# Kernel tuning notes

Hardware: AMD Instinct MI355X
Metric: run time of the kernel (lower is better)

The kernel has to match this reference:

```python
import jax, jax.numpy as jnp
import numpy as np

D_K = 64

def setup_inputs() -> dict:
    key = jax.random.key(0)
    kq, kk, kv, km = jax.random.split(key, 4)
    B, H, S, D = 2, 16, 2048, D_K
    q = jax.random.normal(kq, (B, H, S, D), dtype=jnp.float32)
    k = jax.random.normal(kk, (B, H, S, D), dtype=jnp.float32)
    v = jax.random.normal(kv, (B, H, S, D), dtype=jnp.float32)
    atten_mask = jax.random.bernoulli(km, 0.1, (B, H, S, S))  # True = masked out
    return {"q": q, "k": k, "v": v, "atten_mask": atten_mask}

def reference(q, k, v, atten_mask):
    # score = q @ k^T / sqrt(d_k)  -> [B, H, S, S]
    score = jnp.einsum("bhqd,bhkd->bhqk", q, k) / np.sqrt(D_K).astype(np.float32)
    score = jnp.where(atten_mask, jnp.float32(-1e9), score)
    attn = jax.nn.softmax(score, axis=-1)
    return attn  # original module stops before the AV matmul (v unused)
```

## Files before the change

### kernel.cpp

```cpp
#include <hip/hip_runtime.h>

typedef _Float16 f16x8 __attribute__((ext_vector_type(8)));
typedef _Float16 f16x4 __attribute__((ext_vector_type(4)));
typedef float    f32x4 __attribute__((ext_vector_type(4)));
typedef int      i32x4 __attribute__((ext_vector_type(4)));

#define S_LEN 2048
#define D_KH  64
#define NBH   32
#define QTILE 16
#define NBLK  (NBH * (S_LEN / QTILE))
#define THREADS 512
#define QK_ELEMS (NBH * S_LEN * D_KH)

__device__ __forceinline__ f16x8 cvt8(const float4 a, const float4 b) {
  f16x8 r;
  r[0] = (_Float16)a.x; r[1] = (_Float16)a.y;
  r[2] = (_Float16)a.z; r[3] = (_Float16)a.w;
  r[4] = (_Float16)b.x; r[5] = (_Float16)b.y;
  r[6] = (_Float16)b.z; r[7] = (_Float16)b.w;
  return r;
}

__global__ __launch_bounds__(256) void cvt_qk_kernel(
    const float* __restrict__ q, const float* __restrict__ kmat,
    _Float16* __restrict__ qh, _Float16* __restrict__ kh) {
  const long long idx = ((long long)blockIdx.x * 256 + threadIdx.x) * 8;
  float4 q0 = *(const float4*)(q + idx);
  float4 q1 = *(const float4*)(q + idx + 4);
  const float s = 0.125f;
  q0.x *= s; q0.y *= s; q0.z *= s; q0.w *= s;
  q1.x *= s; q1.y *= s; q1.z *= s; q1.w *= s;
  *(f16x8*)(qh + idx) = cvt8(q0, q1);
  const float4 k0 = *(const float4*)(kmat + idx);
  const float4 k1 = *(const float4*)(kmat + idx + 4);
  *(f16x8*)(kh + idx) = cvt8(k0, k1);
}

__device__ __forceinline__ void softmax_row(float sv[32], const int l,
                                            float* __restrict__ op) {
  float mx = -3.0e38f;
  #pragma unroll
  for (int i = 0; i < 32; ++i) mx = fmaxf(mx, sv[i]);
  #pragma unroll
  for (int off = 32; off > 0; off >>= 1)
    mx = fmaxf(mx, __shfl_xor(mx, off, 64));
  float sum = 0.f;
  #pragma unroll
  for (int i = 0; i < 32; ++i) { sv[i] = __expf(sv[i] - mx); sum += sv[i]; }
  #pragma unroll
  for (int off = 32; off > 0; off >>= 1)
    sum += __shfl_xor(sum, off, 64);
  const float inv = 1.0f / sum;
  #pragma unroll
  for (int i = 0; i < 8; ++i) {
    const int col = (i << 8) + (l << 2);
    f32x4 o = { sv[4 * i + 0] * inv, sv[4 * i + 1] * inv,
                sv[4 * i + 2] * inv, sv[4 * i + 3] * inv };
    __builtin_nontemporal_store(o, (f32x4*)(op + col));
  }
}

template <bool F16>
__global__ __launch_bounds__(THREADS, 4) void sdpa_probs_kernel(
    const float* __restrict__ qf, const float* __restrict__ kf,
    const _Float16* __restrict__ qh, const _Float16* __restrict__ kh,
    const int* __restrict__ mask, float* __restrict__ out) {
  const int bid = (int)blockIdx.x;
  const int nb  = (bid & 7) * (NBLK / 8) + (bid >> 3);
  const int bh  = nb >> 7;
  const int qt  = nb & 127;

  __shared__ _Float16 sc[QTILE][S_LEN];

  const int tid   = (int)threadIdx.x;
  const int w     = tid >> 6;
  const int l     = tid & 63;
  const int lo    = l & 15;
  const int g     = l >> 4;
  const int dbase = g << 3;

  const size_t qk_bh = (size_t)bh * S_LEN * D_KH;
  const size_t obh   = (size_t)bh * S_LEN * S_LEN;

  const int rowA = w << 1, rowB = rowA + 1;
  const size_t orowA = obh + (size_t)(qt * QTILE + rowA) * S_LEN;
  const size_t orowB = obh + (size_t)(qt * QTILE + rowB) * S_LEN;

  i32x4 mA[8];
  {
    const int* mrow = mask + orowA;
    #pragma unroll
    for (int i = 0; i < 8; ++i)
      mA[i] = __builtin_nontemporal_load((const i32x4*)(mrow + (i << 8) + (l << 2)));
  }

  f16x8 a0, a1;
  if constexpr (F16) {
    const _Float16* qp = qh + qk_bh + (size_t)(qt * QTILE + lo) * D_KH + dbase;
    a0 = *(const f16x8*)qp;
    a1 = *(const f16x8*)(qp + 32);
  } else {
    const float* qp = qf + qk_bh + (size_t)(qt * QTILE + lo) * D_KH;
    float4 t0 = *(const float4*)(qp + dbase);
    float4 t1 = *(const float4*)(qp + dbase + 4);
    float4 t2 = *(const float4*)(qp + dbase + 32);
    float4 t3 = *(const float4*)(qp + dbase + 36);
    const float s = 0.125f;
    t0.x *= s; t0.y *= s; t0.z *= s; t0.w *= s;
    t1.x *= s; t1.y *= s; t1.z *= s; t1.w *= s;
    t2.x *= s; t2.y *= s; t2.z *= s; t2.w *= s;
    t3.x *= s; t3.y *= s; t3.z *= s; t3.w *= s;
    a0 = cvt8(t0, t1);
    a1 = cvt8(t2, t3);
  }

  #pragma unroll 4
  for (int kt = 0; kt < 16; ++kt) {
    const int kcol = (w << 8) + (kt << 4) + lo;
    f16x8 b0, b1;
    if constexpr (F16) {
      const _Float16* kp = kh + qk_bh + (size_t)kcol * D_KH + dbase;
      b0 = *(const f16x8*)kp;
      b1 = *(const f16x8*)(kp + 32);
    } else {
      const float* kp = kf + qk_bh + (size_t)kcol * D_KH + dbase;
      b0 = cvt8(*(const float4*)(kp), *(const float4*)(kp + 4));
      b1 = cvt8(*(const float4*)(kp + 32), *(const float4*)(kp + 36));
    }
    f32x4 acc = {0.f, 0.f, 0.f, 0.f};
    acc = __builtin_amdgcn_mfma_f32_16x16x32_f16(a0, b0, acc, 0, 0, 0);
    acc = __builtin_amdgcn_mfma_f32_16x16x32_f16(a1, b1, acc, 0, 0, 0);
    const int phys = kcol ^ (g << 4);
    #pragma unroll
    for (int r = 0; r < 4; ++r)
      sc[(g << 2) + r][phys] = (_Float16)acc[r];
  }

  #pragma unroll
  for (int i = 0; i < 8; ++i) asm volatile("" :: "v"(mA[i]));
  __syncthreads();

  const int physx = (w >> 1) << 4;
  float sv[32];
  #pragma unroll
  for (int i = 0; i < 8; ++i) {
    const int col = (i << 8) + (l << 2);
    const f16x4 h = *(const f16x4*)&sc[rowA][col ^ physx];
    sv[4 * i + 0] = mA[i].x ? -1.0e9f : (float)h[0];
    sv[4 * i + 1] = mA[i].y ? -1.0e9f : (float)h[1];
    sv[4 * i + 2] = mA[i].z ? -1.0e9f : (float)h[2];
    sv[4 * i + 3] = mA[i].w ? -1.0e9f : (float)h[3];
  }
  i32x4 mB[8];
  {
    const int* mrow = mask + orowB;
    #pragma unroll
    for (int i = 0; i < 8; ++i)
      mB[i] = __builtin_nontemporal_load((const i32x4*)(mrow + (i << 8) + (l << 2)));
  }
  softmax_row(sv, l, out + orowA);

  #pragma unroll
  for (int i = 0; i < 8; ++i) {
    const int col = (i << 8) + (l << 2);
    const f16x4 h = *(const f16x4*)&sc[rowB][col ^ physx];
    sv[4 * i + 0] = mB[i].x ? -1.0e9f : (float)h[0];
    sv[4 * i + 1] = mB[i].y ? -1.0e9f : (float)h[1];
    sv[4 * i + 2] = mB[i].z ? -1.0e9f : (float)h[2];
    sv[4 * i + 3] = mB[i].w ? -1.0e9f : (float)h[3];
  }
  softmax_row(sv, l, out + orowB);
}

extern "C" void kernel_launch(void* const* d_in, const int* in_sizes, int n_in,
                              void* d_out, int out_size, void* d_ws, size_t ws_size,
                              hipStream_t stream) {
  const float* q    = (const float*)d_in[0];
  const float* kmat = (const float*)d_in[1];
  const int*   mask = (const int*)d_in[3];
  float*       out  = (float*)d_out;

  const size_t need = (size_t)QK_ELEMS * 2 * sizeof(_Float16);
  if (ws_size >= need) {
    _Float16* qh = (_Float16*)d_ws;
    _Float16* kh = qh + QK_ELEMS;
    cvt_qk_kernel<<<dim3(QK_ELEMS / 8 / 256), dim3(256), 0, stream>>>(q, kmat, qh, kh);
    sdpa_probs_kernel<true><<<dim3(NBLK), dim3(THREADS), 0, stream>>>(
        nullptr, nullptr, qh, kh, mask, out);
  } else {
    sdpa_probs_kernel<false><<<dim3(NBLK), dim3(THREADS), 0, stream>>>(
        q, kmat, nullptr, nullptr, mask, out);
  }
}
```

Before: 238.8 us.

## Keep scores in registers via transposed MFMA and cross-wave softmax reduction

```diff
diff --git a/kernel.cpp b/kernel.cpp
--- a/kernel.cpp
+++ b/kernel.cpp
@@ -1,7 +1,6 @@
 #include <hip/hip_runtime.h>
 
 typedef _Float16 f16x8 __attribute__((ext_vector_type(8)));
-typedef _Float16 f16x4 __attribute__((ext_vector_type(4)));
 typedef float    f32x4 __attribute__((ext_vector_type(4)));
 typedef int      i32x4 __attribute__((ext_vector_type(4)));
 
@@ -37,32 +36,8 @@
   *(f16x8*)(kh + idx) = cvt8(k0, k1);
 }
 
-__device__ __forceinline__ void softmax_row(float sv[32], const int l,
-                                            float* __restrict__ op) {
-  float mx = -3.0e38f;
-  #pragma unroll
-  for (int i = 0; i < 32; ++i) mx = fmaxf(mx, sv[i]);
-  #pragma unroll
-  for (int off = 32; off > 0; off >>= 1)
-    mx = fmaxf(mx, __shfl_xor(mx, off, 64));
-  float sum = 0.f;
-  #pragma unroll
-  for (int i = 0; i < 32; ++i) { sv[i] = __expf(sv[i] - mx); sum += sv[i]; }
-  #pragma unroll
-  for (int off = 32; off > 0; off >>= 1)
-    sum += __shfl_xor(sum, off, 64);
-  const float inv = 1.0f / sum;
-  #pragma unroll
-  for (int i = 0; i < 8; ++i) {
-    const int col = (i << 8) + (l << 2);
-    f32x4 o = { sv[4 * i + 0] * inv, sv[4 * i + 1] * inv,
-                sv[4 * i + 2] * inv, sv[4 * i + 3] * inv };
-    __builtin_nontemporal_store(o, (f32x4*)(op + col));
-  }
-}
-
 template <bool F16>
-__global__ __launch_bounds__(THREADS, 4) void sdpa_probs_kernel(
+__global__ __launch_bounds__(THREADS, 3) void sdpa_probs_kernel(
     const float* __restrict__ qf, const float* __restrict__ kf,
     const _Float16* __restrict__ qh, const _Float16* __restrict__ kh,
     const int* __restrict__ mask, float* __restrict__ out) {
@@ -71,106 +46,97 @@
   const int bh  = nb >> 7;
   const int qt  = nb & 127;
 
-  __shared__ _Float16 sc[QTILE][S_LEN];
+  __shared__ float smax[8][16];
+  __shared__ float ssum[8][16];
 
-  const int tid   = (int)threadIdx.x;
-  const int w     = tid >> 6;
-  const int l     = tid & 63;
-  const int lo    = l & 15;
-  const int g     = l >> 4;
-  const int dbase = g << 3;
+  const int tid = (int)threadIdx.x;
+  const int w   = tid >> 6;
+  const int l   = tid & 63;
+  const int lo  = l & 15;
+  const int g   = l >> 4;
 
   const size_t qk_bh = (size_t)bh * S_LEN * D_KH;
   const size_t obh   = (size_t)bh * S_LEN * S_LEN;
+  const int    qrow  = qt * QTILE + lo;
+  const size_t orow  = obh + (size_t)qrow * S_LEN;
+  const int    cbase = (w << 8) + (g << 2);
 
-  const int rowA = w << 1, rowB = rowA + 1;
-  const size_t orowA = obh + (size_t)(qt * QTILE + rowA) * S_LEN;
-  const size_t orowB = obh + (size_t)(qt * QTILE + rowB) * S_LEN;
-
-  i32x4 mA[8];
-  {
-    const int* mrow = mask + orowA;
-    #pragma unroll
-    for (int i = 0; i < 8; ++i)
-      mA[i] = __builtin_nontemporal_load((const i32x4*)(mrow + (i << 8) + (l << 2)));
-  }
-
-  f16x8 a0, a1;
+  f16x8 qb0, qb1;
   if constexpr (F16) {
-    const _Float16* qp = qh + qk_bh + (size_t)(qt * QTILE + lo) * D_KH + dbase;
-    a0 = *(const f16x8*)qp;
-    a1 = *(const f16x8*)(qp + 32);
+    const _Float16* qp = qh + qk_bh + (size_t)qrow * D_KH + (g << 3);
+    qb0 = *(const f16x8*)qp;
+    qb1 = *(const f16x8*)(qp + 32);
   } else {
-    const float* qp = qf + qk_bh + (size_t)(qt * QTILE + lo) * D_KH;
-    float4 t0 = *(const float4*)(qp + dbase);
-    float4 t1 = *(const float4*)(qp + dbase + 4);
-    float4 t2 = *(const float4*)(qp + dbase + 32);
-    float4 t3 = *(const float4*)(qp + dbase + 36);
+    const float* qp = qf + qk_bh + (size_t)qrow * D_KH + (g << 3);
+    float4 t0 = *(const float4*)(qp);
+    float4 t1 = *(const float4*)(qp + 4);
+    float4 t2 = *(const float4*)(qp + 32);
+    float4 t3 = *(const float4*)(qp + 36);
     const float s = 0.125f;
     t0.x *= s; t0.y *= s; t0.z *= s; t0.w *= s;
     t1.x *= s; t1.y *= s; t1.z *= s; t1.w *= s;
     t2.x *= s; t2.y *= s; t2.z *= s; t2.w *= s;
     t3.x *= s; t3.y *= s; t3.z *= s; t3.w *= s;
-    a0 = cvt8(t0, t1);
-    a1 = cvt8(t2, t3);
+    qb0 = cvt8(t0, t1);
+    qb1 = cvt8(t2, t3);
   }
 
-  #pragma unroll 4
+  float sv[64];
+  float mx = -3.0e38f;
+  const int* mrow = mask + orow + cbase;
+  #pragma unroll
   for (int kt = 0; kt < 16; ++kt) {
-    const int kcol = (w << 8) + (kt << 4) + lo;
-    f16x8 b0, b1;
+    const int keyA = (w << 8) + (kt << 4) + lo;
+    f16x8 ka0, ka1;
     if constexpr (F16) {
-      const _Float16* kp = kh + qk_bh + (size_t)kcol * D_KH + dbase;
-      b0 = *(const f16x8*)kp;
-      b1 = *(const f16x8*)(kp + 32);
+      const _Float16* kp = kh + qk_bh + (size_t)keyA * D_KH + (g << 3);
+      ka0 = *(const f16x8*)kp;
+      ka1 = *(const f16x8*)(kp + 32);
     } else {
-      const float* kp = kf + qk_bh + (size_t)kcol * D_KH + dbase;
-      b0 = cvt8(*(const float4*)(kp), *(const float4*)(kp + 4));
-      b1 = cvt8(*(const float4*)(kp + 32), *(const float4*)(kp + 36));
+      const float* kp = kf + qk_bh + (size_t)keyA * D_KH + (g << 3);
+      ka0 = cvt8(*(const float4*)(kp), *(const float4*)(kp + 4));
+      ka1 = cvt8(*(const float4*)(kp + 32), *(const float4*)(kp + 36));
     }
+    const i32x4 mv = __builtin_nontemporal_load((const i32x4*)(mrow + (kt << 4)));
     f32x4 acc = {0.f, 0.f, 0.f, 0.f};
-    acc = __builtin_amdgcn_mfma_f32_16x16x32_f16(a0, b0, acc, 0, 0, 0);
-    acc = __builtin_amdgcn_mfma_f32_16x16x32_f16(a1, b1, acc, 0, 0, 0);
-    const int phys = kcol ^ (g << 4);
-    #pragma unroll
-    for (int r = 0; r < 4; ++r)
-      sc[(g << 2) + r][phys] = (_Float16)acc[r];
+    acc = __builtin_amdgcn_mfma_f32_16x16x32_f16(ka0, qb0, acc, 0, 0, 0);
+    acc = __builtin_amdgcn_mfma_f32_16x16x32_f16(ka1, qb1, acc, 0, 0, 0);
+    const float s0 = mv.x ? -1.0e9f : acc[0];
+    const float s1 = mv.y ? -1.0e9f : acc[1];
+    const float s2 = mv.z ? -1.0e9f : acc[2];
+    const float s3 = mv.w ? -1.0e9f : acc[3];
+    sv[4 * kt + 0] = s0; sv[4 * kt + 1] = s1;
+    sv[4 * kt + 2] = s2; sv[4 * kt + 3] = s3;
+    mx = fmaxf(mx, fmaxf(fmaxf(s0, s1), fmaxf(s2, s3)));
   }
 
+  mx = fmaxf(mx, __shfl_xor(mx, 16, 64));
+  mx = fmaxf(mx, __shfl_xor(mx, 32, 64));
+  if (l < 16) smax[w][l] = mx;
+  __syncthreads();
+  float gmx = smax[0][lo];
   #pragma unroll
-  for (int i = 0; i < 8; ++i) asm volatile("" :: "v"(mA[i]));
+  for (int j = 1; j < 8; ++j) gmx = fmaxf(gmx, smax[j][lo]);
+
+  float sum = 0.f;
+  #pragma unroll
+  for (int i = 0; i < 64; ++i) { sv[i] = __expf(sv[i] - gmx); sum += sv[i]; }
+  sum += __shfl_xor(sum, 16, 64);
+  sum += __shfl_xor(sum, 32, 64);
+  if (l < 16) ssum[w][l] = sum;
   __syncthreads();
+  float tot = ssum[0][lo];
+  #pragma unroll
+  for (int j = 1; j < 8; ++j) tot += ssum[j][lo];
+  const float inv = 1.0f / tot;
 
-  const int physx = (w >> 1) << 4;
-  float sv[32];
+  float* op = out + orow + cbase;
   #pragma unroll
-  for (int i = 0; i < 8; ++i) {
-    const int col = (i << 8) + (l << 2);
-    const f16x4 h = *(const f16x4*)&sc[rowA][col ^ physx];
-    sv[4 * i + 0] = mA[i].x ? -1.0e9f : (float)h[0];
-    sv[4 * i + 1] = mA[i].y ? -1.0e9f : (float)h[1];
-    sv[4 * i + 2] = mA[i].z ? -1.0e9f : (float)h[2];
-    sv[4 * i + 3] = mA[i].w ? -1.0e9f : (float)h[3];
+  for (int kt = 0; kt < 16; ++kt) {
+    f32x4 o = { sv[4 * kt + 0] * inv, sv[4 * kt + 1] * inv,
+                sv[4 * kt + 2] * inv, sv[4 * kt + 3] * inv };
+    __builtin_nontemporal_store(o, (f32x4*)(op + (kt << 4)));
   }
-  i32x4 mB[8];
-  {
-    const int* mrow = mask + orowB;
-    #pragma unroll
-    for (int i = 0; i < 8; ++i)
-      mB[i] = __builtin_nontemporal_load((const i32x4*)(mrow + (i << 8) + (l << 2)));
-  }
-  softmax_row(sv, l, out + orowA);
-
-  #pragma unroll
-  for (int i = 0; i < 8; ++i) {
-    const int col = (i << 8) + (l << 2);
-    const f16x4 h = *(const f16x4*)&sc[rowB][col ^ physx];
-    sv[4 * i + 0] = mB[i].x ? -1.0e9f : (float)h[0];
-    sv[4 * i + 1] = mB[i].y ? -1.0e9f : (float)h[1];
-    sv[4 * i + 2] = mB[i].z ? -1.0e9f : (float)h[2];
-    sv[4 * i + 3] = mB[i].w ? -1.0e9f : (float)h[3];
-  }
-  softmax_row(sv, l, out + orowB);
 }
 
 extern "C" void kernel_launch(void* const* d_in, const int* in_sizes, int n_in,
```

Measured after the change: 381.6 us. +59.8%, slower.

## Fold row max into MFMA loop and stage exponentials in LDS

Applied to the files above, without the earlier changes.

```diff
diff --git a/kernel.cpp b/kernel.cpp
--- a/kernel.cpp
+++ b/kernel.cpp
@@ -37,30 +37,6 @@
   *(f16x8*)(kh + idx) = cvt8(k0, k1);
 }
 
-__device__ __forceinline__ void softmax_row(float sv[32], const int l,
-                                            float* __restrict__ op) {
-  float mx = -3.0e38f;
-  #pragma unroll
-  for (int i = 0; i < 32; ++i) mx = fmaxf(mx, sv[i]);
-  #pragma unroll
-  for (int off = 32; off > 0; off >>= 1)
-    mx = fmaxf(mx, __shfl_xor(mx, off, 64));
-  float sum = 0.f;
-  #pragma unroll
-  for (int i = 0; i < 32; ++i) { sv[i] = __expf(sv[i] - mx); sum += sv[i]; }
-  #pragma unroll
-  for (int off = 32; off > 0; off >>= 1)
-    sum += __shfl_xor(sum, off, 64);
-  const float inv = 1.0f / sum;
-  #pragma unroll
-  for (int i = 0; i < 8; ++i) {
-    const int col = (i << 8) + (l << 2);
-    f32x4 o = { sv[4 * i + 0] * inv, sv[4 * i + 1] * inv,
-                sv[4 * i + 2] * inv, sv[4 * i + 3] * inv };
-    __builtin_nontemporal_store(o, (f32x4*)(op + col));
-  }
-}
-
 template <bool F16>
 __global__ __launch_bounds__(THREADS, 4) void sdpa_probs_kernel(
     const float* __restrict__ qf, const float* __restrict__ kf,
@@ -72,6 +48,7 @@
   const int qt  = nb & 127;
 
   __shared__ _Float16 sc[QTILE][S_LEN];
+  __shared__ float smax[8][QTILE];
 
   const int tid   = (int)threadIdx.x;
   const int w     = tid >> 6;
@@ -89,10 +66,10 @@
 
   i32x4 mA[8];
   {
-    const int* mrow = mask + orowA;
+    const int* mp = mask + orowA + (l << 2);
     #pragma unroll
     for (int i = 0; i < 8; ++i)
-      mA[i] = __builtin_nontemporal_load((const i32x4*)(mrow + (i << 8) + (l << 2)));
+      mA[i] = __builtin_nontemporal_load((const i32x4*)(mp + (i << 8)));
   }
 
   f16x8 a0, a1;
@@ -115,6 +92,7 @@
     a1 = cvt8(t2, t3);
   }
 
+  f32x4 rm = {-3.0e38f, -3.0e38f, -3.0e38f, -3.0e38f};
   #pragma unroll 4
   for (int kt = 0; kt < 16; ++kt) {
     const int kcol = (w << 8) + (kt << 4) + lo;
@@ -131,6 +109,8 @@
     f32x4 acc = {0.f, 0.f, 0.f, 0.f};
     acc = __builtin_amdgcn_mfma_f32_16x16x32_f16(a0, b0, acc, 0, 0, 0);
     acc = __builtin_amdgcn_mfma_f32_16x16x32_f16(a1, b1, acc, 0, 0, 0);
+    rm[0] = fmaxf(rm[0], acc[0]); rm[1] = fmaxf(rm[1], acc[1]);
+    rm[2] = fmaxf(rm[2], acc[2]); rm[3] = fmaxf(rm[3], acc[3]);
     const int phys = kcol ^ (g << 4);
     #pragma unroll
     for (int r = 0; r < 4; ++r)
@@ -138,39 +118,99 @@
   }
 
   #pragma unroll
+  for (int c = 0; c < 4; ++c) {
+    float v = rm[c];
+    v = fmaxf(v, __shfl_xor(v, 1, 64));
+    v = fmaxf(v, __shfl_xor(v, 2, 64));
+    v = fmaxf(v, __shfl_xor(v, 4, 64));
+    v = fmaxf(v, __shfl_xor(v, 8, 64));
+    rm[c] = v;
+  }
+  if (lo == 0) {
+    smax[w][(g << 2) + 0] = rm[0];
+    smax[w][(g << 2) + 1] = rm[1];
+    smax[w][(g << 2) + 2] = rm[2];
+    smax[w][(g << 2) + 3] = rm[3];
+  }
+
+  #pragma unroll
   for (int i = 0; i < 8; ++i) asm volatile("" :: "v"(mA[i]));
   __syncthreads();
 
+  i32x4 mB[8];
+  {
+    const int* mp = mask + orowB + (l << 2);
+    #pragma unroll
+    for (int i = 0; i < 8; ++i)
+      mB[i] = __builtin_nontemporal_load((const i32x4*)(mp + (i << 8)));
+  }
+
+  float gA = smax[0][rowA], gB = smax[0][rowB];
+  #pragma unroll
+  for (int j = 1; j < 8; ++j) {
+    gA = fmaxf(gA, smax[j][rowA]);
+    gB = fmaxf(gB, smax[j][rowB]);
+  }
+
   const int physx = (w >> 1) << 4;
-  float sv[32];
+
+  float sum = 0.f;
+  #pragma unroll
+  for (int i = 0; i < 8; ++i) {
+    const int off = (((i << 8) + (l << 2))) ^ physx;
+    const f16x4 h = *(const f16x4*)&sc[rowA][off];
+    const float e0 = mA[i].x ? 0.f : __expf((float)h[0] - gA);
+    const float e1 = mA[i].y ? 0.f : __expf((float)h[1] - gA);
+    const float e2 = mA[i].z ? 0.f : __expf((float)h[2] - gA);
+    const float e3 = mA[i].w ? 0.f : __expf((float)h[3] - gA);
+    sum += (e0 + e1) + (e2 + e3);
+    f16x4 eh; eh[0] = (_Float16)e0; eh[1] = (_Float16)e1;
+    eh[2] = (_Float16)e2; eh[3] = (_Float16)e3;
+    *(f16x4*)&sc[rowA][off] = eh;
+  }
+  #pragma unroll
+  for (int off = 32; off > 0; off >>= 1)
+    sum += __shfl_xor(sum, off, 64);
+  const float invA = 1.0f / sum;
+
+  float* opA = out + orowA;
   #pragma unroll
   for (int i = 0; i < 8; ++i) {
     const int col = (i << 8) + (l << 2);
     const f16x4 h = *(const f16x4*)&sc[rowA][col ^ physx];
-    sv[4 * i + 0] = mA[i].x ? -1.0e9f : (float)h[0];
-    sv[4 * i + 1] = mA[i].y ? -1.0e9f : (float)h[1];
-    sv[4 * i + 2] = mA[i].z ? -1.0e9f : (float)h[2];
-    sv[4 * i + 3] = mA[i].w ? -1.0e9f : (float)h[3];
-  }
-  i32x4 mB[8];
-  {
-    const int* mrow = mask + orowB;
-    #pragma unroll
-    for (int i = 0; i < 8; ++i)
-      mB[i] = __builtin_nontemporal_load((const i32x4*)(mrow + (i << 8) + (l << 2)));
-  }
-  softmax_row(sv, l, out + orowA);
-
+    f32x4 o = { (float)h[0] * invA, (float)h[1] * invA,
+                (float)h[2] * invA, (float)h[3] * invA };
+    __builtin_nontemporal_store(o, (f32x4*)(opA + col));
+  }
+
+  sum = 0.f;
+  #pragma unroll
+  for (int i = 0; i < 8; ++i) {
+    const int off = (((i << 8) + (l << 2))) ^ physx;
+    const f16x4 h = *(const f16x4*)&sc[rowB][off];
+    const float e0 = mB[i].x ? 0.f : __expf((float)h[0] - gB);
+    const float e1 = mB[i].y ? 0.f : __expf((float)h[1] - gB);
+    const float e2 = mB[i].z ? 0.f : __expf((float)h[2] - gB);
+    const float e3 = mB[i].w ? 0.f : __expf((float)h[3] - gB);
+    sum += (e0 + e1) + (e2 + e3);
+    f16x4 eh; eh[0] = (_Float16)e0; eh[1] = (_Float16)e1;
+    eh[2] = (_Float16)e2; eh[3] = (_Float16)e3;
+    *(f16x4*)&sc[rowB][off] = eh;
+  }
+  #pragma unroll
+  for (int off = 32; off > 0; off >>= 1)
+    sum += __shfl_xor(sum, off, 64);
+  const float invB = 1.0f / sum;
+
+  float* opB = out + orowB;
   #pragma unroll
   for (int i = 0; i < 8; ++i) {
     const int col = (i << 8) + (l << 2);
     const f16x4 h = *(const f16x4*)&sc[rowB][col ^ physx];
-    sv[4 * i + 0] = mB[i].x ? -1.0e9f : (float)h[0];
-    sv[4 * i + 1] = mB[i].y ? -1.0e9f : (float)h[1];
-    sv[4 * i + 2] = mB[i].z ? -1.0e9f : (float)h[2];
-    sv[4 * i + 3] = mB[i].w ? -1.0e9f : (float)h[3];
-  }
-  softmax_row(sv, l, out + orowB);
+    f32x4 o = { (float)h[0] * invB, (float)h[1] * invB,
+                (float)h[2] * invB, (float)h[3] * invB };
+    __builtin_nontemporal_store(o, (f32x4*)(opB + col));
+  }
 }
 
 extern "C" void kernel_launch(void* const* d_in, const int* in_sizes, int n_in,
```

After: 253.7 us. +6.3%, slower.
